# Performance work log

Hardware: AMD Instinct MI355X
Metric: run time of the kernel (lower is better)

Reference implementation:

```python
import jax, jax.numpy as jnp
import numpy as np

DIM = 768
NUM_HEADS = 8
HEAD_DIM = DIM // NUM_HEADS
SCALE = HEAD_DIM ** -0.5


def setup_inputs() -> dict:
    key = jax.random.key(0)
    k1, k2, k3, k4 = jax.random.split(key, 4)
    B, C, H, W = 8, DIM, 32, 32
    x = jax.random.normal(k1, (B, C, H, W), dtype=jnp.float32)
    # torch Linear stores weight as (out, in); y = x @ W.T + b
    w_qkv = jax.random.normal(k2, (3 * DIM, DIM), dtype=jnp.float32) * (DIM ** -0.5)
    w_proj = jax.random.normal(k3, (DIM, DIM), dtype=jnp.float32) * (DIM ** -0.5)
    b_proj = jax.random.normal(k4, (DIM,), dtype=jnp.float32) * 0.02
    return {"x": x, "w_qkv": w_qkv, "w_proj": w_proj, "b_proj": b_proj}


def reference(x, w_qkv, w_proj, b_proj):
    B, C, H, W = x.shape
    N = H * W
    nh, hd = NUM_HEADS, HEAD_DIM
    # (B, C, H, W) -> (B, N, C)
    tokens = x.reshape(B, C, N).transpose(0, 2, 1)
    qkv = tokens @ w_qkv.T  # (B, N, 3C), no bias (qkv_bias=False)
    qkv = qkv.reshape(B, N, 3, nh, hd).transpose(2, 0, 3, 1, 4)  # (3, B, nh, N, hd)
    q, k, v = qkv[0], qkv[1], qkv[2]
    attn = jnp.einsum('bhnd,bhmd->bhnm', q, k) * SCALE
    attn = jax.nn.softmax(attn, axis=-1)  # attn_drop=0.0 (eval)
    out = jnp.einsum('bhnm,bhmd->bhnd', attn, v)  # (B, nh, N, hd)
    out = out.transpose(0, 2, 1, 3).reshape(B, N, C)
    out = out @ w_proj.T + b_proj  # proj_drop=0.0
    return out.transpose(0, 2, 1).reshape(B, C, H, W)
```

## Files before the change

kernel.cpp:

```cpp
#include <hip/hip_runtime.h>

typedef short s16x8 __attribute__((ext_vector_type(8)));
typedef short s16x4 __attribute__((ext_vector_type(4)));
typedef float f32x4 __attribute__((ext_vector_type(4)));
typedef int   i32x4 __attribute__((ext_vector_type(4)));

#define SCALE_F 0.10206207261596577f

__device__ __forceinline__ unsigned short f2bf(float f) {
  unsigned u = __builtin_bit_cast(unsigned, f);
  u += 0x7fffu + ((u >> 16) & 1u);
  return (unsigned short)(u >> 16);
}
__device__ __forceinline__ unsigned pack_bf2(float a, float b) {
  return (unsigned)f2bf(a) | ((unsigned)f2bf(b) << 16);
}

#define MFMA16(a, b, c) __builtin_amdgcn_mfma_f32_16x16x32_bf16((a), (b), (c), 0, 0, 0)

__device__ __forceinline__ void gl_lds16(const unsigned short* g, unsigned short* l) {
  __builtin_amdgcn_global_load_lds(
      (const __attribute__((address_space(1))) void*)g,
      (__attribute__((address_space(3))) void*)l, 16, 0, 0);
}

__global__ __launch_bounds__(256) void cvt_bf16_kernel(const float* __restrict__ src,
                                                       unsigned short* __restrict__ dst, int n4) {
  int i = blockIdx.x * 256 + threadIdx.x;
  if (i >= n4) return;
  f32x4 v = reinterpret_cast<const f32x4*>(src)[i];
  s16x4 o;
  o[0] = (short)f2bf(v[0]); o[1] = (short)f2bf(v[1]);
  o[2] = (short)f2bf(v[2]); o[3] = (short)f2bf(v[3]);
  reinterpret_cast<s16x4*>(dst)[i] = o;
}

__global__ __launch_bounds__(256) void transpose_x_kernel(const float* __restrict__ x,
                                                          unsigned short* __restrict__ tokens) {
  __shared__ float t[32][33];
  const int ct = blockIdx.x * 32, nt = blockIdx.y * 32, b = blockIdx.z;
  const int tx = threadIdx.x, ty = threadIdx.y;
  const float* xp = x + (size_t)b * 768 * 1024;
#pragma unroll
  for (int r = 0; r < 4; ++r) {
    int c = ty + r * 8;
    t[c][tx] = xp[(size_t)(ct + c) * 1024 + nt + tx];
  }
  __syncthreads();
  unsigned short* tp = tokens + (size_t)b * 1024 * 768;
#pragma unroll
  for (int r = 0; r < 4; ++r) {
    int n = ty + r * 8;
    tp[(size_t)(nt + n) * 768 + ct + tx] = f2bf(t[tx][n]);
  }
}


__device__ __forceinline__ void stage128(const unsigned short* __restrict__ A,
                                         const unsigned short* __restrict__ Bt,
                                         unsigned short* lA, unsigned short* lB,
                                         int m0, int n0, int k0, int tid, int wave) {
  const int r2 = tid >> 2, s = tid & 3;
#pragma unroll
  for (int i = 0; i < 2; ++i) {
    const int row = i * 64 + r2;
    const int c = s ^ ((row >> 1) & 3);
    gl_lds16(A + (size_t)(m0 + row) * 768 + k0 + c * 8, lA + i * 2048 + wave * 512);
    gl_lds16(Bt + (size_t)(n0 + row) * 768 + k0 + c * 8, lB + i * 2048 + wave * 512);
  }
}

#define GEMM128_LOOP(A, Bt)                                                             \
  stage128(A, Bt, lA, lB, m0, n0, 0, tid, wave);                                        \
  __syncthreads();                                                                      \
  for (int t = 0; t < 24; ++t) {                                                        \
    const int cur = t & 1;                                                              \
    if (t < 23)                                                                         \
      stage128(A, Bt, lA + (cur ^ 1) * 4096, lB + (cur ^ 1) * 4096, m0, n0,             \
               (t + 1) * 32, tid, wave);                                                \
    s16x8 af[4], bf[4];                                                                 \
    _Pragma("unroll")                                                                   \
    for (int mi = 0; mi < 4; ++mi) {                                                    \
      const int row = wr * 64 + mi * 16 + lr;                                           \
      af[mi] = *reinterpret_cast<const s16x8*>(                                         \
          &lA[cur * 4096 + row * 32 + ((lg ^ ((row >> 1) & 3)) * 8)]);                  \
    }                                                                                   \
    _Pragma("unroll")                                                                   \
    for (int ni = 0; ni < 4; ++ni) {                                                    \
      const int row = wc * 64 + ni * 16 + lr;                                           \
      bf[ni] = *reinterpret_cast<const s16x8*>(                                         \
          &lB[cur * 4096 + row * 32 + ((lg ^ ((row >> 1) & 3)) * 8)]);                  \
    }                                                                                   \
    _Pragma("unroll")                                                                   \
    for (int mi = 0; mi < 4; ++mi)                                                      \
      _Pragma("unroll")                                                                 \
      for (int ni = 0; ni < 4; ++ni)                                                    \
        acc[mi][ni] = MFMA16(af[mi], bf[ni], acc[mi][ni]);                              \
    __syncthreads();                                                                    \
  }

__global__ __launch_bounds__(256, 4) void qkv_gemm_kernel(const unsigned short* __restrict__ A,
                                                          const unsigned short* __restrict__ Bt,
                                                          unsigned short* __restrict__ Qo,
                                                          unsigned short* __restrict__ Ko,
                                                          unsigned short* __restrict__ Vt) {
  __shared__ unsigned short lds_all[16384];
  unsigned short* lA = lds_all;
  unsigned short* lB = lds_all + 8192;

  const int tid = threadIdx.x;
  const int wave = tid >> 6, lane = tid & 63;
  const int wr = wave >> 1, wc = wave & 1;
  const int lr = lane & 15, lg = lane >> 4;
  const int bid = blockIdx.x;
  const int xcd = bid & 7, idx = bid >> 3;
  const int m0 = (xcd * 8 + idx / 18) * 128;
  const int n0 = (idx % 18) * 128;

  f32x4 acc[4][4] = {};
  GEMM128_LOOP(A, Bt)

  const int colbase = n0 + wc * 64;
  const int ttype = colbase / 768;
  if (ttype == 2) {
#pragma unroll
    for (int ni = 0; ni < 4; ++ni) {
      const int cc = colbase + ni * 16 + lr - 2 * 768;
      const int h = cc / 96, d = cc - h * 96;
#pragma unroll
      for (int mi = 0; mi < 4; ++mi) {
        const int gm = m0 + wr * 64 + mi * 16 + lg * 4;
        const int b = gm >> 10, n = gm & 1023;
        s16x4 v;
#pragma unroll
        for (int j = 0; j < 4; ++j) v[j] = (short)f2bf(acc[mi][ni][j]);
        *reinterpret_cast<s16x4*>(Vt + ((size_t)(b * 8 + h) * 96 + d) * 1024 + n) = v;
      }
    }
  } else {
    unsigned short* W = lds_all + wave * 4096;
    unsigned short* dstbuf = (ttype == 0) ? Qo : Ko;
#pragma unroll
    for (int mi = 0; mi < 4; ++mi)
#pragma unroll
      for (int ni = 0; ni < 4; ++ni) {
        const int cc = ni * 16 + lr;
        const int ch = cc >> 3, wi = cc & 7;
#pragma unroll
        for (int j = 0; j < 4; ++j) {
          const int r = mi * 16 + lg * 4 + j;
          W[r * 64 + ((ch ^ (r & 7)) * 8) + wi] = f2bf(acc[mi][ni][j]);
        }
      }
    asm volatile("s_waitcnt lgkmcnt(0)" ::: "memory");
    __builtin_amdgcn_sched_barrier(0);
#pragma unroll
    for (int i = 0; i < 8; ++i) {
      const int r = i * 8 + (lane >> 3), c = lane & 7;
      s16x8 v8 = *reinterpret_cast<const s16x8*>(&W[r * 64 + ((c ^ (r & 7)) * 8)]);
      const int cc = colbase + c * 8 - ttype * 768;
      const int h = cc / 96, d = cc - h * 96;
      const int gm = m0 + wr * 64 + r;
      const int b = gm >> 10, n = gm & 1023;
      *reinterpret_cast<s16x8*>(dstbuf + ((size_t)(b * 8 + h) * 1024 + n) * 96 + d) = v8;
    }
  }
}

__global__ __launch_bounds__(256, 4) void proj_gemm_kernel(const unsigned short* __restrict__ A,
                                                           const unsigned short* __restrict__ Bt,
                                                           const float* __restrict__ bias,
                                                           float* __restrict__ out) {
  __shared__ unsigned short lds_all[16384];
  unsigned short* lA = lds_all;
  unsigned short* lB = lds_all + 8192;

  const int tid = threadIdx.x;
  const int wave = tid >> 6, lane = tid & 63;
  const int wr = wave >> 1, wc = wave & 1;
  const int lr = lane & 15, lg = lane >> 4;
  const int bid = blockIdx.x;
  const int xcd = bid & 7, idx = bid >> 3;
  const int m0 = (xcd * 8 + idx / 6) * 128;
  const int n0 = (idx % 6) * 128;

  f32x4 acc[4][4] = {};
  GEMM128_LOOP(A, Bt)

#pragma unroll
  for (int ni = 0; ni < 4; ++ni) {
    const int col = n0 + wc * 64 + ni * 16 + lr;
    const float bv = bias[col];
#pragma unroll
    for (int mi = 0; mi < 4; ++mi) {
      const int gm = m0 + wr * 64 + mi * 16 + lg * 4;
      const int b = gm >> 10, n = gm & 1023;
      f32x4 v;
#pragma unroll
      for (int j = 0; j < 4; ++j) v[j] = acc[mi][ni][j] + bv;
      *reinterpret_cast<f32x4*>(out + (size_t)b * 768 * 1024 + (size_t)col * 1024 + n) = v;
    }
  }
}

__global__ __launch_bounds__(512, 4) void attn_kernel(const unsigned short* __restrict__ Q,
                                                      const unsigned short* __restrict__ K,
                                                      const unsigned short* __restrict__ Vt,
                                                      unsigned short* __restrict__ Ao) {
  __shared__ unsigned short lds[2][12288];

  const int f = blockIdx.x;
  const int xcd = f & 7;
  const int g = (f >> 3) + xcd * 64;
  const int bh = g >> 3, qb = g & 7;

  const int tid = threadIdx.x, wave = tid >> 6, lane = tid & 63;
  const int lr = lane & 15, lg = lane >> 4;
  const int klo = (lr >> 1) & 3;

  const unsigned short* Qp = Q + (size_t)bh * 1024 * 96;
  const unsigned short* Kp = K + (size_t)bh * 1024 * 96;
  const unsigned short* Vp = Vt + (size_t)bh * 96 * 1024;

  const int qrow = qb * 128 + wave * 16 + lr;
  s16x8 qreg[3];
#pragma unroll
  for (int kd = 0; kd < 3; ++kd)
    qreg[kd] = *reinterpret_cast<const s16x8*>(Qp + (size_t)qrow * 96 + kd * 32 + lg * 8);

  float m_r = -1e30f, l_r = 0.f;
  f32x4 oacc[6] = {};

  const int srcA = lr + ((lg & 1) << 5);
  const int srcB = srcA + 16;
  const bool hiT = (lg & 2) != 0;

#define STAGE(bufi, kv0)                                                              \
  {                                                                                   \
    _Pragma("unroll")                                                                 \
    for (int i = 0; i < 3; ++i) {                                                     \
      const int wl = wave + 8 * i;                                                    \
      if (wl < 12) {                                                                  \
        const int kd = wl >> 2, rg = wl & 3;                                          \
        const int row = rg * 16 + (lane >> 2);                                        \
        const int c8 = (lane & 3) ^ ((row >> 1) & 3);                                 \
        gl_lds16(Kp + (size_t)((kv0) + row) * 96 + kd * 32 + c8 * 8,                  \
                 &lds[bufi][0] + kd * 2048 + rg * 512);                               \
      } else {                                                                        \
        const int v = wl - 12;                                                        \
        const int gs = v / 6, rg = v - gs * 6;                                        \
        const int drow = rg * 16 + (lane >> 2);                                       \
        const int c8 = (lane & 3) ^ ((drow >> 1) & 3);                                \
        gl_lds16(Vp + (size_t)drow * 1024 + (kv0) + gs * 32 + c8 * 8,                 \
                 &lds[bufi][0] + 6144 + gs * 3072 + rg * 512);                        \
      }                                                                               \
    }                                                                                 \
  }

  STAGE(0, 0);
  __syncthreads();

  for (int gt = 0; gt < 16; ++gt) {
    const int buf = gt & 1;
    if (gt < 15) STAGE(buf ^ 1, (gt + 1) * 64);

    f32x4 sacc[4] = {};
#pragma unroll
    for (int c = 0; c < 4; ++c) {
#pragma unroll
      for (int kd = 0; kd < 3; ++kd) {
        s16x8 kf = *reinterpret_cast<const s16x8*>(
            &lds[buf][kd * 2048 + (c * 16 + lr) * 32 + ((lg ^ klo) * 8)]);
        sacc[c] = MFMA16(kf, qreg[kd], sacc[c]);
      }
    }

    float mx = -1e30f;
#pragma unroll
    for (int c = 0; c < 4; ++c) {
#pragma unroll
      for (int j = 0; j < 4; ++j) {
        sacc[c][j] *= SCALE_F;
        mx = fmaxf(mx, sacc[c][j]);
      }
    }
    mx = fmaxf(mx, __shfl_xor(mx, 16));
    mx = fmaxf(mx, __shfl_xor(mx, 32));
    if (!__all(mx - m_r <= 8.0f)) {
      const float mNew = fmaxf(m_r, mx);
      const float rsc = __expf(m_r - mNew);
      l_r *= rsc;
#pragma unroll
      for (int dt = 0; dt < 6; ++dt) oacc[dt] *= rsc;
      m_r = mNew;
    }
    float ts = 0.f;
    unsigned pk[4][2];
#pragma unroll
    for (int c = 0; c < 4; ++c) {
      float p0 = __expf(sacc[c][0] - m_r);
      float p1 = __expf(sacc[c][1] - m_r);
      float p2 = __expf(sacc[c][2] - m_r);
      float p3 = __expf(sacc[c][3] - m_r);
      ts += (p0 + p1) + (p2 + p3);
      pk[c][0] = pack_bf2(p0, p1);
      pk[c][1] = pack_bf2(p2, p3);
    }
    ts += __shfl_xor(ts, 16);
    ts += __shfl_xor(ts, 32);
    l_r += ts;

#pragma unroll
    for (int gs = 0; gs < 2; ++gs) {
      const int t0 = gs * 2, t1 = t0 + 1;
      int la0 = __shfl((int)pk[t0][0], srcA), la1 = __shfl((int)pk[t1][0], srcA);
      int ha0 = __shfl((int)pk[t0][1], srcA), ha1 = __shfl((int)pk[t1][1], srcA);
      int lb0 = __shfl((int)pk[t0][0], srcB), lb1 = __shfl((int)pk[t1][0], srcB);
      int hb0 = __shfl((int)pk[t0][1], srcB), hb1 = __shfl((int)pk[t1][1], srcB);
      i32x4 bi;
      bi[0] = hiT ? la1 : la0;
      bi[1] = hiT ? ha1 : ha0;
      bi[2] = hiT ? lb1 : lb0;
      bi[3] = hiT ? hb1 : hb0;
      s16x8 pf = __builtin_bit_cast(s16x8, bi);
#pragma unroll
      for (int dt = 0; dt < 6; ++dt) {
        s16x8 vf = *reinterpret_cast<const s16x8*>(
            &lds[buf][6144 + gs * 3072 + (dt * 16 + lr) * 32 + ((lg ^ klo) * 8)]);
        oacc[dt] = MFMA16(vf, pf, oacc[dt]);
      }
    }
    __syncthreads();
  }

  const float invl = 1.0f / l_r;
  const int b_ = bh >> 3, h_ = bh & 7;
  unsigned short* orow = Ao + (size_t)(b_ * 1024 + qrow) * 768 + h_ * 96;
#pragma unroll
  for (int dt = 0; dt < 6; ++dt) {
    s16x4 o4;
#pragma unroll
    for (int j = 0; j < 4; ++j) o4[j] = (short)f2bf(oacc[dt][j] * invl);
    *reinterpret_cast<s16x4*>(orow + dt * 16 + lg * 4) = o4;
  }
#undef STAGE
}

extern "C" void kernel_launch(void* const* d_in, const int* in_sizes, int n_in,
                              void* d_out, int out_size, void* d_ws, size_t ws_size,
                              hipStream_t stream) {
  const float* x = (const float*)d_in[0];
  const float* wqkv = (const float*)d_in[1];
  const float* wproj = (const float*)d_in[2];
  const float* bproj = (const float*)d_in[3];
  float* out = (float*)d_out;

  unsigned short* ws = (unsigned short*)d_ws;
  unsigned short* tokens = ws;
  unsigned short* wqkv_b = tokens + 8192 * 768;
  unsigned short* wproj_b = wqkv_b + 2304 * 768;
  unsigned short* Qb = wproj_b + 768 * 768;
  unsigned short* Kb = Qb + 64 * 1024 * 96;
  unsigned short* Vb = Kb + 64 * 1024 * 96;
  unsigned short* Ab = Vb + 64 * 1024 * 96;

  cvt_bf16_kernel<<<1728, 256, 0, stream>>>(wqkv, wqkv_b, 2304 * 768 / 4);
  cvt_bf16_kernel<<<576, 256, 0, stream>>>(wproj, wproj_b, 768 * 768 / 4);
  transpose_x_kernel<<<dim3(24, 32, 8), dim3(32, 8), 0, stream>>>(x, tokens);
  qkv_gemm_kernel<<<1152, 256, 0, stream>>>(tokens, wqkv_b, Qb, Kb, Vb);
  attn_kernel<<<512, 512, 0, stream>>>(Qb, Kb, Vb, Ab);
  proj_gemm_kernel<<<384, 256, 0, stream>>>(Ab, wproj_b, bproj, out);
}
```

Baseline: 130.0 us.

## Permute V layout to drop P shuffles, use exp2 and packed bf16 converts

The QKV GEMM epilogue now writes V^T with a permuted token order within each 32-token group. This lets the attention kernel feed its packed softmax probabilities straight into the PV MFMA without cross-lane shuffles. Softmax folds the scale and log2e into one FMA before a raw v_exp_f32, conversions use the hardware v_cvt_pk_bf16_f32 instruction, and s_setprio is raised around the MFMA blocks. The goal is to cut VALU and shuffle work in the attention inner loop, but it depends on the V permutation matching the MFMA operand layout exactly.

```diff
diff --git a/kernel.cpp b/kernel.cpp
--- a/kernel.cpp
+++ b/kernel.cpp
@@ -4,16 +4,26 @@
 typedef short s16x4 __attribute__((ext_vector_type(4)));
 typedef float f32x4 __attribute__((ext_vector_type(4)));
 typedef int   i32x4 __attribute__((ext_vector_type(4)));
+typedef unsigned u32x2 __attribute__((ext_vector_type(2)));
 
 #define SCALE_F 0.10206207261596577f
+#define KLOG2E  0.14724444f
+#define DEFER_THR 11.5415603f
 
 __device__ __forceinline__ unsigned short f2bf(float f) {
   unsigned u = __builtin_bit_cast(unsigned, f);
   u += 0x7fffu + ((u >> 16) & 1u);
   return (unsigned short)(u >> 16);
 }
-__device__ __forceinline__ unsigned pack_bf2(float a, float b) {
-  return (unsigned)f2bf(a) | ((unsigned)f2bf(b) << 16);
+__device__ __forceinline__ unsigned cvt_pk_bf16(float a, float b) {
+  unsigned r;
+  asm("v_cvt_pk_bf16_f32 %0, %1, %2" : "=v"(r) : "v"(a), "v"(b));
+  return r;
+}
+__device__ __forceinline__ float exp2_fast(float x) {
+  float r;
+  asm("v_exp_f32 %0, %1" : "=v"(r) : "v"(x));
+  return r;
 }
 
 #define MFMA16(a, b, c) __builtin_amdgcn_mfma_f32_16x16x32_bf16((a), (b), (c), 0, 0, 0)
@@ -54,7 +64,6 @@
     tp[(size_t)(nt + n) * 768 + ct + tx] = f2bf(t[tx][n]);
   }
 }
-
 
 __device__ __forceinline__ void stage128(const unsigned short* __restrict__ A,
                                          const unsigned short* __restrict__ Bt,
@@ -131,10 +140,12 @@
       for (int mi = 0; mi < 4; ++mi) {
         const int gm = m0 + wr * 64 + mi * 16 + lg * 4;
         const int b = gm >> 10, n = gm & 1023;
-        s16x4 v;
-#pragma unroll
-        for (int j = 0; j < 4; ++j) v[j] = (short)f2bf(acc[mi][ni][j]);
-        *reinterpret_cast<s16x4*>(Vt + ((size_t)(b * 8 + h) * 96 + d) * 1024 + n) = v;
+        const int np = (n & ~31) | (((n >> 2) & 3) << 3) | (((n >> 4) & 1) << 2);
+        u32x2 p2;
+        p2[0] = cvt_pk_bf16(acc[mi][ni][0], acc[mi][ni][1]);
+        p2[1] = cvt_pk_bf16(acc[mi][ni][2], acc[mi][ni][3]);
+        *reinterpret_cast<s16x4*>(Vt + ((size_t)(b * 8 + h) * 96 + d) * 1024 + np) =
+            __builtin_bit_cast(s16x4, p2);
       }
     }
   } else {
@@ -228,12 +239,8 @@
   for (int kd = 0; kd < 3; ++kd)
     qreg[kd] = *reinterpret_cast<const s16x8*>(Qp + (size_t)qrow * 96 + kd * 32 + lg * 8);
 
-  float m_r = -1e30f, l_r = 0.f;
+  float m2 = -1e30f, l_r = 0.f;
   f32x4 oacc[6] = {};
-
-  const int srcA = lr + ((lg & 1) << 5);
-  const int srcB = srcA + 16;
-  const bool hiT = (lg & 2) != 0;
 
 #define STAGE(bufi, kv0)                                                              \
   {                                                                                   \
@@ -265,6 +272,7 @@
     if (gt < 15) STAGE(buf ^ 1, (gt + 1) * 64);
 
     f32x4 sacc[4] = {};
+    __builtin_amdgcn_s_setprio(1);
 #pragma unroll
     for (int c = 0; c < 4; ++c) {
 #pragma unroll
@@ -274,54 +282,47 @@
         sacc[c] = MFMA16(kf, qreg[kd], sacc[c]);
       }
     }
-
-    float mx = -1e30f;
-#pragma unroll
-    for (int c = 0; c < 4; ++c) {
-#pragma unroll
-      for (int j = 0; j < 4; ++j) {
-        sacc[c][j] *= SCALE_F;
-        mx = fmaxf(mx, sacc[c][j]);
-      }
-    }
+    __builtin_amdgcn_s_setprio(0);
+
+    float mx = fmaxf(fmaxf(sacc[0][0], sacc[0][1]), fmaxf(sacc[0][2], sacc[0][3]));
+#pragma unroll
+    for (int c = 1; c < 4; ++c)
+      mx = fmaxf(mx, fmaxf(fmaxf(sacc[c][0], sacc[c][1]), fmaxf(sacc[c][2], sacc[c][3])));
     mx = fmaxf(mx, __shfl_xor(mx, 16));
     mx = fmaxf(mx, __shfl_xor(mx, 32));
-    if (!__all(mx - m_r <= 8.0f)) {
-      const float mNew = fmaxf(m_r, mx);
-      const float rsc = __expf(m_r - mNew);
+    const float mc = mx * KLOG2E;
+    if (!__all(mc - m2 <= DEFER_THR)) {
+      const float m2n = fmaxf(m2, mc);
+      const float rsc = exp2_fast(m2 - m2n);
       l_r *= rsc;
 #pragma unroll
       for (int dt = 0; dt < 6; ++dt) oacc[dt] *= rsc;
-      m_r = mNew;
+      m2 = m2n;
     }
     float ts = 0.f;
     unsigned pk[4][2];
 #pragma unroll
     for (int c = 0; c < 4; ++c) {
-      float p0 = __expf(sacc[c][0] - m_r);
-      float p1 = __expf(sacc[c][1] - m_r);
-      float p2 = __expf(sacc[c][2] - m_r);
-      float p3 = __expf(sacc[c][3] - m_r);
+      float p0 = exp2_fast(__builtin_fmaf(sacc[c][0], KLOG2E, -m2));
+      float p1 = exp2_fast(__builtin_fmaf(sacc[c][1], KLOG2E, -m2));
+      float p2 = exp2_fast(__builtin_fmaf(sacc[c][2], KLOG2E, -m2));
+      float p3 = exp2_fast(__builtin_fmaf(sacc[c][3], KLOG2E, -m2));
       ts += (p0 + p1) + (p2 + p3);
-      pk[c][0] = pack_bf2(p0, p1);
-      pk[c][1] = pack_bf2(p2, p3);
+      pk[c][0] = cvt_pk_bf16(p0, p1);
+      pk[c][1] = cvt_pk_bf16(p2, p3);
     }
     ts += __shfl_xor(ts, 16);
     ts += __shfl_xor(ts, 32);
     l_r += ts;
 
+    __builtin_amdgcn_s_setprio(1);
 #pragma unroll
     for (int gs = 0; gs < 2; ++gs) {
-      const int t0 = gs * 2, t1 = t0 + 1;
-      int la0 = __shfl((int)pk[t0][0], srcA), la1 = __shfl((int)pk[t1][0], srcA);
-      int ha0 = __shfl((int)pk[t0][1], srcA), ha1 = __shfl((int)pk[t1][1], srcA);
-      int lb0 = __shfl((int)pk[t0][0], srcB), lb1 = __shfl((int)pk[t1][0], srcB);
-      int hb0 = __shfl((int)pk[t0][1], srcB), hb1 = __shfl((int)pk[t1][1], srcB);
       i32x4 bi;
-      bi[0] = hiT ? la1 : la0;
-      bi[1] = hiT ? ha1 : ha0;
-      bi[2] = hiT ? lb1 : lb0;
-      bi[3] = hiT ? hb1 : hb0;
+      bi[0] = (int)pk[2 * gs][0];
+      bi[1] = (int)pk[2 * gs][1];
+      bi[2] = (int)pk[2 * gs + 1][0];
+      bi[3] = (int)pk[2 * gs + 1][1];
       s16x8 pf = __builtin_bit_cast(s16x8, bi);
 #pragma unroll
       for (int dt = 0; dt < 6; ++dt) {
@@ -330,6 +331,7 @@
         oacc[dt] = MFMA16(vf, pf, oacc[dt]);
       }
     }
+    __builtin_amdgcn_s_setprio(0);
     __syncthreads();
   }
 
@@ -338,10 +340,10 @@
   unsigned short* orow = Ao + (size_t)(b_ * 1024 + qrow) * 768 + h_ * 96;
 #pragma unroll
   for (int dt = 0; dt < 6; ++dt) {
-    s16x4 o4;
-#pragma unroll
-    for (int j = 0; j < 4; ++j) o4[j] = (short)f2bf(oacc[dt][j] * invl);
-    *reinterpret_cast<s16x4*>(orow + dt * 16 + lg * 4) = o4;
+    u32x2 p2;
+    p2[0] = cvt_pk_bf16(oacc[dt][0] * invl, oacc[dt][1] * invl);
+    p2[1] = cvt_pk_bf16(oacc[dt][2] * invl, oacc[dt][3] * invl);
+    *reinterpret_cast<s16x4*>(orow + dt * 16 + lg * 4) = __builtin_bit_cast(s16x4, p2);
   }
 #undef STAGE
 }
```

Result: faster. 119.1 us (-8.4%).
